# Kernel optimization log

Hardware: AMD Instinct MI355X
Metric: run time of the kernel (lower is better)

Reference implementation:

```python
import jax, jax.numpy as jnp
import numpy as np

S, B, C = 56, 5, 20
N = 128


def _cxcywh_to_xyxy(b):
    cx, cy, w, h = b[..., 0], b[..., 1], b[..., 2], b[..., 3]
    return jnp.stack([cx - 0.5 * w, cy - 0.5 * h, cx + 0.5 * w, cy + 0.5 * h], axis=-1)


def setup_inputs() -> dict:
    key = jax.random.key(0)
    k1, k2, k3 = jax.random.split(key, 3)
    predicts_tensor = jax.random.normal(k1, (N, S, S, B, C + 5), dtype=jnp.float32)
    targets_tensor = jax.random.uniform(k2, (N, S, S, C + 5), dtype=jnp.float32)
    anchors = jax.random.uniform(k3, (B, 2), dtype=jnp.float32)
    return {"predicts_tensor": predicts_tensor, "targets_tensor": targets_tensor, "anchors": anchors}


def reference(predicts_tensor, targets_tensor, anchors):
    p = predicts_tensor.reshape(-1, S, S, B, C + 5)
    # decode: sigmoid on cx,cy ; exp * anchor on w,h
    xy = jax.nn.sigmoid(p[..., C + 1:C + 3])
    wh = jnp.exp(p[..., C + 3:]) * anchors  # anchors [B,2] broadcasts over [...,B,2]
    p = jnp.concatenate([p[..., :C + 1], xy, wh], axis=-1)

    pb = _cxcywh_to_xyxy(p[..., C + 1:])                         # [N,S,S,B,4]
    tb = _cxcywh_to_xyxy(targets_tensor[..., C + 1:])[..., None, :]  # [N,S,S,1,4]

    # torchvision box_iou, vectorized over all cells and B boxes
    lt = jnp.maximum(pb[..., :2], tb[..., :2])
    rb = jnp.minimum(pb[..., 2:], tb[..., 2:])
    whi = jnp.clip(rb - lt, 0.0)
    inter = whi[..., 0] * whi[..., 1]
    area_p = (pb[..., 2] - pb[..., 0]) * (pb[..., 3] - pb[..., 1])
    area_t = (tb[..., 2] - tb[..., 0]) * (tb[..., 3] - tb[..., 1])
    ious = inter / (area_p + area_t - inter)                     # [N,S,S,B]

    best_idx = jnp.argmax(ious, axis=-1)                         # [N,S,S]
    pbest = jnp.take_along_axis(p, best_idx[..., None, None], axis=3)[..., 0, :]  # [N,S,S,C+5]
    pbest = pbest.at[..., 0].set(pbest[..., 0] * best_idx.astype(pbest.dtype))

    exists = targets_tensor[..., C:C + 1]
    sse = lambda a, b: jnp.sum((a - b) ** 2)  # MSELoss(reduction='sum')

    loss_xcyc = sse(exists * pbest[..., C + 1:C + 3], exists * targets_tensor[..., C + 1:C + 3])
    p_wh = pbest[..., C + 3:]
    p_wh = jnp.sign(p_wh) * jnp.sqrt(jnp.abs(p_wh) + 1e-6)
    loss_wh = sse(exists * p_wh, exists * targets_tensor[..., C + 3:])
    loss_cls = sse(exists * pbest[..., :C], exists * targets_tensor[..., :C])
    loss_obj = sse(exists * pbest[..., C:C + 1], exists * targets_tensor[..., C:C + 1])
    noobj = 1.0 - exists
    loss_noobj = sse(noobj * pbest[..., C:C + 1], noobj * targets_tensor[..., C:C + 1])

    return loss_xcyc + loss_wh + loss_cls + loss_noobj + loss_obj
```

## Files before the change

### kernel.cpp

```cpp
#include <hip/hip_runtime.h>

constexpr int S_   = 56;
constexpr int B_   = 5;
constexpr int C_   = 20;
constexpr int N_   = 128;
constexpr int CELLS = N_ * S_ * S_;
constexpr int PSTR  = B_ * (C_ + 5);
constexpr int TSTR  = C_ + 5;

__global__ __launch_bounds__(256) void yolo_loss_kernel(
    const float* __restrict__ pred,
    const float* __restrict__ targ,
    const float* __restrict__ anch,
    float* __restrict__ out)
{
    const int cell = blockIdx.x * 256 + threadIdx.x;
    float local = 0.f;

    if (cell < CELLS) {
        const float* p = pred + (long)cell * PSTR;
        const float* t = targ + (long)cell * TSTR;

        float tc[TSTR];
        #pragma unroll
        for (int k = 0; k < TSTR; ++k) tc[k] = t[k];

        const float tcx = tc[C_ + 1], tcy = tc[C_ + 2];
        const float tw  = tc[C_ + 3], th  = tc[C_ + 4];
        const float tx0 = tcx - 0.5f * tw, ty0 = tcy - 0.5f * th;
        const float tx1 = tcx + 0.5f * tw, ty1 = tcy + 0.5f * th;
        const float area_t = tw * th;

        float best_iou = -1.f;
        int   best_b = 0;
        float bcx = 0.f, bcy = 0.f, bw = 0.f, bh = 0.f;

        #pragma unroll
        for (int b = 0; b < B_; ++b) {
            const float rcx = p[b * TSTR + C_ + 1];
            const float rcy = p[b * TSTR + C_ + 2];
            const float rw  = p[b * TSTR + C_ + 3];
            const float rh  = p[b * TSTR + C_ + 4];

            const float cx = __builtin_amdgcn_rcpf(1.f + __expf(-rcx));
            const float cy = __builtin_amdgcn_rcpf(1.f + __expf(-rcy));
            const float w  = __expf(rw) * anch[2 * b];
            const float h  = __expf(rh) * anch[2 * b + 1];

            const float x0 = cx - 0.5f * w, y0 = cy - 0.5f * h;
            const float x1 = cx + 0.5f * w, y1 = cy + 0.5f * h;

            float wi = fminf(x1, tx1) - fmaxf(x0, tx0);
            float hi = fminf(y1, ty1) - fmaxf(y0, ty0);
            wi = fmaxf(wi, 0.f);
            hi = fmaxf(hi, 0.f);
            const float inter = wi * hi;
            const float iou = inter * __builtin_amdgcn_rcpf(w * h + area_t - inter);

            if (iou > best_iou) {
                best_iou = iou; best_b = b;
                bcx = cx; bcy = cy; bw = w; bh = h;
            }
        }

        const float* pb = p + best_b * TSTR;

        float acc = 0.f;
        #pragma unroll
        for (int k = 0; k < C_; ++k) {
            float v = pb[k];
            if (k == 0) v *= (float)best_b;
            const float d = v - tc[k];
            acc = fmaf(d, d, acc);
        }

        float d;
        d = bcx - tcx; acc = fmaf(d, d, acc);
        d = bcy - tcy; acc = fmaf(d, d, acc);

        d = sqrtf(bw + 1e-6f) - tw; acc = fmaf(d, d, acc);
        d = sqrtf(bh + 1e-6f) - th; acc = fmaf(d, d, acc);

        const float e    = tc[C_];
        const float ne   = 1.f - e;
        const float dobj = pb[C_] - e;
        local = e * e * acc + (e * e + ne * ne) * (dobj * dobj);
    }

    #pragma unroll
    for (int off = 32; off > 0; off >>= 1)
        local += __shfl_down(local, off, 64);

    __shared__ float wsum[4];
    const int lane = threadIdx.x & 63;
    const int wid  = threadIdx.x >> 6;
    if (lane == 0) wsum[wid] = local;
    __syncthreads();
    if (threadIdx.x == 0)
        atomicAdd(out, wsum[0] + wsum[1] + wsum[2] + wsum[3]);
}

extern "C" void kernel_launch(void* const* d_in, const int* in_sizes, int n_in,
                              void* d_out, int out_size, void* d_ws, size_t ws_size,
                              hipStream_t stream) {
    const float* pred = (const float*)d_in[0];
    const float* targ = (const float*)d_in[1];
    const float* anch = (const float*)d_in[2];
    float* out = (float*)d_out;

    hipMemsetAsync(out, 0, (size_t)out_size * sizeof(float), stream);

    const int blocks = (CELLS + 255) / 256;
    yolo_loss_kernel<<<blocks, 256, 0, stream>>>(pred, targ, anch, out);
}
```

Baseline: 310.0 us.

## Stage cell data via coalesced global-to-LDS loads and spread atomics over buckets

Each 64-thread block now copies its 64 cells of predictions and targets into LDS with coalesced 16-byte direct global-to-LDS loads, replacing the strided per-thread global reads. The partial sums go to 64 padded buckets in workspace instead of one address, and a small finalize kernel adds them up. This aims to fix uncoalesced memory access and atomic contention on a single address. In exchange it needs about 38 KB of LDS per block, which limits occupancy, adds an extra kernel launch, and reads LDS with a large per-thread stride that may cause bank conflicts.

```diff
diff --git a/kernel.cpp b/kernel.cpp
--- a/kernel.cpp
+++ b/kernel.cpp
@@ -8,96 +8,135 @@
 constexpr int PSTR  = B_ * (C_ + 5);
 constexpr int TSTR  = C_ + 5;
 
-__global__ __launch_bounds__(256) void yolo_loss_kernel(
+constexpr int CPB    = 64;
+constexpr int NBLK   = CELLS / CPB;
+constexpr int PRED_B = CPB * PSTR * 4;
+constexpr int TARG_B = CPB * TSTR * 4;
+
+constexpr int NBUCKET       = 64;
+constexpr int BUCKET_STRIDE = 32;
+
+__device__ __forceinline__ void gload_lds16(const char* g, char* l) {
+    __builtin_amdgcn_global_load_lds(
+        (const __attribute__((address_space(1))) void*)g,
+        (__attribute__((address_space(3))) void*)l,
+        16, 0, 0);
+}
+
+__global__ __launch_bounds__(64) void yolo_loss_kernel(
     const float* __restrict__ pred,
     const float* __restrict__ targ,
     const float* __restrict__ anch,
-    float* __restrict__ out)
+    float* __restrict__ buckets)
 {
-    const int cell = blockIdx.x * 256 + threadIdx.x;
-    float local = 0.f;
+    __shared__ char lds[PRED_B + TARG_B];
 
-    if (cell < CELLS) {
-        const float* p = pred + (long)cell * PSTR;
-        const float* t = targ + (long)cell * TSTR;
+    const int lane  = threadIdx.x;
+    const int cell0 = blockIdx.x * CPB;
 
-        float tc[TSTR];
-        #pragma unroll
-        for (int k = 0; k < TSTR; ++k) tc[k] = t[k];
+    const char* gp = (const char*)(pred + (size_t)cell0 * PSTR);
+    const char* gt = (const char*)(targ + (size_t)cell0 * TSTR);
 
-        const float tcx = tc[C_ + 1], tcy = tc[C_ + 2];
-        const float tw  = tc[C_ + 3], th  = tc[C_ + 4];
-        const float tx0 = tcx - 0.5f * tw, ty0 = tcy - 0.5f * th;
-        const float tx1 = tcx + 0.5f * tw, ty1 = tcy + 0.5f * th;
-        const float area_t = tw * th;
+    #pragma unroll
+    for (int it = 0; it < 31; ++it)
+        gload_lds16(gp + it * 1024 + lane * 16, lds + it * 1024);
+    #pragma unroll
+    for (int it = 0; it < 6; ++it)
+        gload_lds16(gt + it * 1024 + lane * 16, lds + PRED_B + it * 1024);
+    if (lane < 16) {
+        gload_lds16(gp + 31744 + lane * 16, lds + 31744);
+        gload_lds16(gt + 6144  + lane * 16, lds + PRED_B + 6144);
+    }
 
-        float best_iou = -1.f;
-        int   best_b = 0;
-        float bcx = 0.f, bcy = 0.f, bw = 0.f, bh = 0.f;
+    float aw[B_], ah[B_];
+    #pragma unroll
+    for (int b = 0; b < B_; ++b) { aw[b] = anch[2 * b]; ah[b] = anch[2 * b + 1]; }
 
-        #pragma unroll
-        for (int b = 0; b < B_; ++b) {
-            const float rcx = p[b * TSTR + C_ + 1];
-            const float rcy = p[b * TSTR + C_ + 2];
-            const float rw  = p[b * TSTR + C_ + 3];
-            const float rh  = p[b * TSTR + C_ + 4];
+    __syncthreads();
 
-            const float cx = __builtin_amdgcn_rcpf(1.f + __expf(-rcx));
-            const float cy = __builtin_amdgcn_rcpf(1.f + __expf(-rcy));
-            const float w  = __expf(rw) * anch[2 * b];
-            const float h  = __expf(rh) * anch[2 * b + 1];
+    const float* pc = (const float*)lds + (size_t)lane * PSTR;
+    const float* tp = (const float*)(lds + PRED_B) + (size_t)lane * TSTR;
 
-            const float x0 = cx - 0.5f * w, y0 = cy - 0.5f * h;
-            const float x1 = cx + 0.5f * w, y1 = cy + 0.5f * h;
+    const float tcx = tp[C_ + 1], tcy = tp[C_ + 2];
+    const float tw  = tp[C_ + 3], th  = tp[C_ + 4];
+    const float tx0 = tcx - 0.5f * tw, ty0 = tcy - 0.5f * th;
+    const float tx1 = tcx + 0.5f * tw, ty1 = tcy + 0.5f * th;
+    const float area_t = tw * th;
 
-            float wi = fminf(x1, tx1) - fmaxf(x0, tx0);
-            float hi = fminf(y1, ty1) - fmaxf(y0, ty0);
-            wi = fmaxf(wi, 0.f);
-            hi = fmaxf(hi, 0.f);
-            const float inter = wi * hi;
-            const float iou = inter * __builtin_amdgcn_rcpf(w * h + area_t - inter);
+    float best_iou = -1.f;
+    int   best_b = 0;
+    float bcx = 0.f, bcy = 0.f, bw = 0.f, bh = 0.f;
 
-            if (iou > best_iou) {
-                best_iou = iou; best_b = b;
-                bcx = cx; bcy = cy; bw = w; bh = h;
-            }
-        }
+    #pragma unroll
+    for (int b = 0; b < B_; ++b) {
+        const float rcx = pc[b * TSTR + C_ + 1];
+        const float rcy = pc[b * TSTR + C_ + 2];
+        const float rw  = pc[b * TSTR + C_ + 3];
+        const float rh  = pc[b * TSTR + C_ + 4];
 
-        const float* pb = p + best_b * TSTR;
+        const float cx = __builtin_amdgcn_rcpf(1.f + __expf(-rcx));
+        const float cy = __builtin_amdgcn_rcpf(1.f + __expf(-rcy));
+        const float w  = __expf(rw) * aw[b];
+        const float h  = __expf(rh) * ah[b];
 
-        float acc = 0.f;
-        #pragma unroll
-        for (int k = 0; k < C_; ++k) {
-            float v = pb[k];
-            if (k == 0) v *= (float)best_b;
-            const float d = v - tc[k];
-            acc = fmaf(d, d, acc);
-        }
+        const float x0 = cx - 0.5f * w, y0 = cy - 0.5f * h;
+        const float x1 = cx + 0.5f * w, y1 = cy + 0.5f * h;
 
-        float d;
-        d = bcx - tcx; acc = fmaf(d, d, acc);
-        d = bcy - tcy; acc = fmaf(d, d, acc);
+        float wi = fminf(x1, tx1) - fmaxf(x0, tx0);
+        float hi = fminf(y1, ty1) - fmaxf(y0, ty0);
+        wi = fmaxf(wi, 0.f);
+        hi = fmaxf(hi, 0.f);
+        const float inter = wi * hi;
+        const float iou = inter * __builtin_amdgcn_rcpf(w * h + area_t - inter);
 
-        d = sqrtf(bw + 1e-6f) - tw; acc = fmaf(d, d, acc);
-        d = sqrtf(bh + 1e-6f) - th; acc = fmaf(d, d, acc);
+        const bool better = iou > best_iou;
+        best_iou = better ? iou : best_iou;
+        best_b   = better ? b   : best_b;
+        bcx = better ? cx : bcx;
+        bcy = better ? cy : bcy;
+        bw  = better ? w  : bw;
+        bh  = better ? h  : bh;
+    }
 
-        const float e    = tc[C_];
-        const float ne   = 1.f - e;
-        const float dobj = pb[C_] - e;
-        local = e * e * acc + (e * e + ne * ne) * (dobj * dobj);
+    const float* pb = pc + best_b * TSTR;
+
+    float acc = 0.f;
+    #pragma unroll
+    for (int k = 0; k < C_; ++k) {
+        float v = pb[k];
+        if (k == 0) v *= (float)best_b;
+        const float d = v - tp[k];
+        acc = fmaf(d, d, acc);
     }
+
+    float d;
+    d = bcx - tcx; acc = fmaf(d, d, acc);
+    d = bcy - tcy; acc = fmaf(d, d, acc);
+
+    d = sqrtf(bw + 1e-6f) - tw; acc = fmaf(d, d, acc);
+    d = sqrtf(bh + 1e-6f) - th; acc = fmaf(d, d, acc);
+
+    const float e    = tp[C_];
+    const float ne   = 1.f - e;
+    const float dobj = pb[C_] - e;
+    float local = e * e * acc + (e * e + ne * ne) * (dobj * dobj);
 
     #pragma unroll
     for (int off = 32; off > 0; off >>= 1)
         local += __shfl_down(local, off, 64);
 
-    __shared__ float wsum[4];
-    const int lane = threadIdx.x & 63;
-    const int wid  = threadIdx.x >> 6;
-    if (lane == 0) wsum[wid] = local;
-    __syncthreads();
-    if (threadIdx.x == 0)
-        atomicAdd(out, wsum[0] + wsum[1] + wsum[2] + wsum[3]);
+    if (lane == 0)
+        atomicAdd(&buckets[(blockIdx.x & (NBUCKET - 1)) * BUCKET_STRIDE], local);
+}
+
+__global__ __launch_bounds__(64) void finalize_kernel(
+    const float* __restrict__ buckets, float* __restrict__ out)
+{
+    float v = buckets[threadIdx.x * BUCKET_STRIDE];
+    #pragma unroll
+    for (int off = 32; off > 0; off >>= 1)
+        v += __shfl_down(v, off, 64);
+    if (threadIdx.x == 0) out[0] = v;
 }
 
 extern "C" void kernel_launch(void* const* d_in, const int* in_sizes, int n_in,
@@ -106,10 +145,11 @@
     const float* pred = (const float*)d_in[0];
     const float* targ = (const float*)d_in[1];
     const float* anch = (const float*)d_in[2];
-    float* out = (float*)d_out;
+    float* out     = (float*)d_out;
+    float* buckets = (float*)d_ws;
 
-    hipMemsetAsync(out, 0, (size_t)out_size * sizeof(float), stream);
+    hipMemsetAsync(buckets, 0, NBUCKET * BUCKET_STRIDE * sizeof(float), stream);
 
-    const int blocks = (CELLS + 255) / 256;
-    yolo_loss_kernel<<<blocks, 256, 0, stream>>>(pred, targ, anch, out);
+    yolo_loss_kernel<<<NBLK, CPB, 0, stream>>>(pred, targ, anch, buckets);
+    finalize_kernel<<<1, 64, 0, stream>>>(buckets, out);
 }
```

After: 302.4 us. 1.03x faster.
